# Optimization experiments

Hardware: AMD Instinct MI355X
Metric: run time of the kernel (lower is better)

## Reference

```python
import jax, jax.numpy as jnp
import numpy as np

HID = 32      # STGAT hidden_dim
HEADS = 8
NHID = HID // HEADS  # per-head hidden = 4
NEG_SLOPE = 0.2


def lstm_layer(x, Wih, Whh, bih, bhh):
    # x: (BN, T, H_in); torch gate order i, f, g, o
    BN = x.shape[0]
    H = Whh.shape[1]
    b = bih + bhh

    def step(carry, xt):
        h, c = carry
        z = xt @ Wih.T + h @ Whh.T + b
        i, f, g, o = jnp.split(z, 4, axis=-1)
        c = jax.nn.sigmoid(f) * c + jax.nn.sigmoid(i) * jnp.tanh(g)
        h = jax.nn.sigmoid(o) * jnp.tanh(c)
        return (h, c), h

    h0 = jnp.zeros((BN, H), x.dtype)
    _, ys = jax.lax.scan(step, (h0, h0), jnp.swapaxes(x, 0, 1))
    return jnp.swapaxes(ys, 0, 1)  # (BN, T, H)


def setup_inputs():
    key = jax.random.key(0)
    ks = jax.random.split(key, 16)
    B, N, T_in, F_in = 8, 300, 12, 3
    T_out, F_out = 12, 3
    X = jax.random.normal(ks[0], (B, N, T_in, F_in), jnp.float32)
    adj = (jax.random.uniform(ks[1], (N, N)) < 0.05).astype(jnp.float32)
    A_hat = jnp.maximum(adj, jnp.eye(N, dtype=jnp.float32))  # self-loops

    def init(k, shape, fan):
        return jax.random.normal(k, shape, jnp.float32) / np.float32(np.sqrt(fan))

    W_gat = init(ks[2], (HID, F_in), F_in)          # linear (no bias)
    a_attn = init(ks[3], (2 * NHID,), 2 * NHID)     # attn (no bias), flattened (1, 2*nhid)
    W_ih0 = init(ks[4], (4 * HID, HID), HID)
    W_hh0 = init(ks[5], (4 * HID, HID), HID)
    b_ih0 = init(ks[6], (4 * HID,), HID)
    b_hh0 = init(ks[7], (4 * HID,), HID)
    W_ih1 = init(ks[8], (4 * HID, HID), HID)
    W_hh1 = init(ks[9], (4 * HID, HID), HID)
    b_ih1 = init(ks[10], (4 * HID,), HID)
    b_hh1 = init(ks[11], (4 * HID,), HID)
    fc_W = init(ks[12], (F_out * T_out, HID), HID)
    fc_b = init(ks[13], (F_out * T_out,), HID)
    return {"A_hat": A_hat, "X": X, "W_gat": W_gat, "a_attn": a_attn,
            "W_ih0": W_ih0, "W_hh0": W_hh0, "b_ih0": b_ih0, "b_hh0": b_hh0,
            "W_ih1": W_ih1, "W_hh1": W_hh1, "b_ih1": b_ih1, "b_hh1": b_hh1,
            "fc_W": fc_W, "fc_b": fc_b}


def reference(A_hat, X, W_gat, a_attn, W_ih0, W_hh0, b_ih0, b_hh0,
              W_ih1, W_hh1, b_ih1, b_hh1, fc_W, fc_b):
    B, N, T, F = X.shape
    T_out = fc_W.shape[0] // F  # nums_feature_output == F here

    # --- GAT, vectorized over (batch, timestep) ---
    # g: (B, N, T, HEADS, NHID)
    g = (X @ W_gat.T).reshape(B, N, T, HEADS, NHID)
    a_l, a_r = a_attn[:NHID], a_attn[NHID:]
    # attn(g_concat) = a_l . g_i + a_r . g_j  (exact split of the concat+linear)
    gl = jnp.einsum('bithd,d->bith', g, a_l)
    gr = jnp.einsum('bjthd,d->bjth', g, a_r)
    e = jax.nn.leaky_relu(gl[:, :, None] + gr[:, None, :], NEG_SLOPE)  # (B,i,j,T,H)
    mask = (A_hat == 0)[None, :, :, None, None]
    e = jnp.where(mask, -jnp.inf, e)
    a = jax.nn.softmax(e, axis=2)  # softmax over j (dim=1 of the (i,j,h) tensor)
    h_gat = jnp.einsum('bijth,bjthd->bithd', a, g).reshape(B, N, T, HID)

    # --- 2-layer LSTM over time, per (b, n) sequence ---
    lstm_in = h_gat.reshape(B * N, T, HID)
    h1 = lstm_layer(lstm_in, W_ih0, W_hh0, b_ih0, b_hh0)
    h2 = lstm_layer(h1, W_ih1, W_hh1, b_ih1, b_hh1)
    h_last = h2[:, -1, :]  # (B*N, HID)

    out = h_last @ fc_W.T + fc_b
    return out.reshape(B, N, T_out, F)
```

## Files before the change

### kernel.cpp

```cpp
#include <hip/hip_runtime.h>

typedef __attribute__((ext_vector_type(8))) short s8v;
typedef __attribute__((ext_vector_type(4))) float f4v;

__device__ __forceinline__ float sgm(float x) { return 1.f / (1.f + __expf(-x)); }
__device__ __forceinline__ float tanh_fast(float x) {
    float e = __expf(-2.f * fabsf(x));
    float t = (1.f - e) / (1.f + e);
    return copysignf(t, x);
}
__device__ __forceinline__ void bsplit(float x, short& hi, short& lo) {
    unsigned u = __float_as_uint(x);
    unsigned hb = u & 0xffff0000u;
    hi = (short)(hb >> 16);
    float r = x - __uint_as_float(hb);
    lo = (short)(__float_as_uint(r) >> 16);
}

#define SQ 5

__device__ __forceinline__ f4v zA(const short* vh, const short* vl,
    const s8v (&ah)[2], const s8v (&al)[2], f4v bias, int boff, int g)
{
    s8v bh0 = *(const s8v*)((const char*)vh + boff +      g*16);
    s8v bh1 = *(const s8v*)((const char*)vh + boff + 64 + g*16);
    s8v bl0 = *(const s8v*)((const char*)vl + boff +      g*16);
    s8v bl1 = *(const s8v*)((const char*)vl + boff + 64 + g*16);
    f4v acc = bias;
    acc = __builtin_amdgcn_mfma_f32_16x16x32_bf16(ah[0], bh0, acc, 0, 0, 0);
    acc = __builtin_amdgcn_mfma_f32_16x16x32_bf16(ah[1], bh1, acc, 0, 0, 0);
    acc = __builtin_amdgcn_mfma_f32_16x16x32_bf16(al[0], bh0, acc, 0, 0, 0);
    acc = __builtin_amdgcn_mfma_f32_16x16x32_bf16(al[1], bh1, acc, 0, 0, 0);
    acc = __builtin_amdgcn_mfma_f32_16x16x32_bf16(ah[0], bl0, acc, 0, 0, 0);
    acc = __builtin_amdgcn_mfma_f32_16x16x32_bf16(ah[1], bl1, acc, 0, 0, 0);
    return acc;
}

__global__ __launch_bounds__(512, 4) void k_stgat(
    const float* __restrict__ A,    const float* __restrict__ X,
    const float* __restrict__ Wg,   const float* __restrict__ aat,
    const float* __restrict__ Wih0, const float* __restrict__ Whh0,
    const float* __restrict__ bih0, const float* __restrict__ bhh0,
    const float* __restrict__ Wih1, const float* __restrict__ Whh1,
    const float* __restrict__ bih1, const float* __restrict__ bhh1,
    const float* __restrict__ fcW,  const float* __restrict__ fcb,
    float* __restrict__ out)
{
    __shared__ int   snbr[SQ][64];
    __shared__ int   scnt[SQ];
    __shared__ float shg[SQ*384];
    __shared__ __align__(16) char uarea[43200];
    const int tid  = threadIdx.x;
    const int w    = tid >> 6;
    const int l    = tid & 63;
    const int seq0 = blockIdx.x * SQ;
    const int b    = seq0 / 300, i0 = seq0 - b*300;

    float* Xs = (float*)uarea;

    {
        const float* Xg = X + (size_t)b * 10800;
        for (int x = tid; x < 10800; x += 512) Xs[x] = Xg[x];
    }
    if (w < SQ) {
        int i = i0 + w;
        int c = 0;
        for (int j0 = 0; j0 < 300; j0 += 64) {
            int j = j0 + l;
            bool p = (j < 300) && (A[i*300 + j] != 0.f);
            unsigned long long m = __ballot(p);
            if (p) {
                int pos = __popcll(m & ((1ull << l) - 1ull));
                if (c + pos < 64) snbr[w][c + pos] = j;
            }
            c += __popcll(m);
        }
        if (c > 64) c = 64;
        if (l == 0) scnt[w] = c;
    }

    const int n16 = l & 15;
    const int g   = l >> 4;
    const int cc  = w*4 + g;
    const int arow = (n16 & 3)*32 + w*4 + (n16 >> 2);
    s8v a0h[2], a0l[2], a1h[2], a1l[2];
    {
        const float* s00 = Wih0 + arow*32 + g*8;
        const float* s01 = Whh0 + arow*32 + g*8;
        const float* s10 = Wih1 + arow*32 + g*8;
        const float* s11 = Whh1 + arow*32 + g*8;
        #pragma unroll
        for (int j = 0; j < 8; j++) {
            short hh, ll;
            bsplit(s00[j], hh, ll); a0h[0][j]=hh; a0l[0][j]=ll;
            bsplit(s01[j], hh, ll); a0h[1][j]=hh; a0l[1][j]=ll;
            bsplit(s10[j], hh, ll); a1h[0][j]=hh; a1l[0][j]=ll;
            bsplit(s11[j], hh, ll); a1h[1][j]=hh; a1l[1][j]=ll;
        }
    }
    f4v bias0, bias1;
    #pragma unroll
    for (int r = 0; r < 4; r++) {
        int br = r*32 + cc;
        bias0[r] = bih0[br] + bhh0[br];
        bias1[r] = bih1[br] + bhh1[br];
    }

    __syncthreads();

    {
        const int h = l >> 3, j8 = l & 7, d = j8 & 3;
        float wal0=0.f, wal1=0.f, wal2=0.f, war0=0.f, war1=0.f, war2=0.f;
        #pragma unroll
        for (int dd = 0; dd < 4; dd++) {
            float av = aat[dd], bv = aat[4+dd];
            const float* wr = Wg + (h*4+dd)*3;
            wal0 += wr[0]*av; wal1 += wr[1]*av; wal2 += wr[2]*av;
            war0 += wr[0]*bv; war1 += wr[1]*bv; war2 += wr[2]*bv;
        }
        const float* wp = Wg + (h*4+d)*3;
        float wp0 = wp[0], wp1 = wp[1], wp2 = wp[2];

        for (int u = w; u < SQ*12; u += 8) {
            int us = u / 12, t = u - us*12;
            int i = i0 + us;
            int c = scnt[us];

            const float* Xi = Xs + i*36 + t*3;
            float gl = Xi[0]*wal0 + Xi[1]*wal1 + Xi[2]*wal2;

            float m = -1e30f, s = 0.f, a0 = 0.f, a1 = 0.f, a2 = 0.f;
            for (int kk = j8; kk < c; kk += 8) {
                int j = snbr[us][kk];
                const float* Xj = Xs + j*36 + t*3;
                float y0 = Xj[0], y1 = Xj[1], y2 = Xj[2];
                float e = gl + y0*war0 + y1*war1 + y2*war2;
                e = e > 0.f ? e : 0.2f*e;
                if (e > m) {
                    float sc = __expf(m - e);
                    s = s*sc + 1.f;
                    a0 = a0*sc + y0; a1 = a1*sc + y1; a2 = a2*sc + y2;
                    m = e;
                } else {
                    float wt = __expf(e - m);
                    s += wt;
                    a0 += wt*y0; a1 += wt*y1; a2 += wt*y2;
                }
            }
            #pragma unroll
            for (int off = 1; off <= 4; off <<= 1) {
                float m2 = __shfl_xor(m, off, 64);
                float s2 = __shfl_xor(s, off, 64);
                float b0 = __shfl_xor(a0, off, 64);
                float b1 = __shfl_xor(a1, off, 64);
                float b2 = __shfl_xor(a2, off, 64);
                float mo = fmaxf(m, m2);
                float w1 = __expf(m - mo), w2 = __expf(m2 - mo);
                s = s*w1 + s2*w2;
                a0 = a0*w1 + b0*w2; a1 = a1*w1 + b1*w2; a2 = a2*w1 + b2*w2;
                m = mo;
            }
            if (j8 < 4)
                shg[us*384 + t*32 + h*4 + d] = (a0*wp0 + a1*wp1 + a2*wp2) / s;
        }
    }
    __syncthreads();

    short* vh0 = (short*)uarea;
    short* vl0 = vh0 + 16*72;
    short* vh1 = vl0 + 16*72;
    short* vl1 = vh1 + 16*72;
    float* sh1f = (float*)(vl1 + 16*72);

    for (int x = tid; x < 16*72; x += 512) {
        vh0[x] = 0; vl0[x] = 0; vh1[x] = 0; vl1[x] = 0;
    }
    __syncthreads();
    if (tid < SQ*32) {
        int us = tid >> 5, uc = tid & 31;
        short hh, ll; bsplit(shg[us*384 + uc], hh, ll);
        vh0[us*72 + uc] = hh;  vl0[us*72 + uc] = ll;
    }
    __syncthreads();

    const int boff = n16 * 144;
    float c0 = 0.f, c1 = 0.f;

    {
        f4v z = zA(vh0, vl0, a0h, a0l, bias0, boff, g);
        __syncthreads();
        c0 = sgm(z[1])*c0 + sgm(z[0])*tanh_fast(z[2]);
        float h0v = sgm(z[3])*tanh_fast(c0);
        short hh, ll; bsplit(h0v, hh, ll);
        vh0[n16*72 + 32 + cc] = hh;  vl0[n16*72 + 32 + cc] = ll;
        vh1[n16*72 + cc]      = hh;  vl1[n16*72 + cc]      = ll;
        if (tid < SQ*32) {
            int us = tid >> 5, uc = tid & 31;
            bsplit(shg[us*384 + 32 + uc], hh, ll);
            vh0[us*72 + uc] = hh;  vl0[us*72 + uc] = ll;
        }
        __syncthreads();
    }

    for (int t = 0; t < 12; t++) {
        f4v z1 = zA(vh1, vl1, a1h, a1l, bias1, boff, g);
        f4v z0;
        if (t < 11)
            z0 = zA(vh0, vl0, a0h, a0l, bias0, boff, g);
        __syncthreads();
        c1 = sgm(z1[1])*c1 + sgm(z1[0])*tanh_fast(z1[2]);
        float h1v = sgm(z1[3])*tanh_fast(c1);
        short hh, ll; bsplit(h1v, hh, ll);
        vh1[n16*72 + 32 + cc] = hh;  vl1[n16*72 + 32 + cc] = ll;
        if (t == 11) {
            if (n16 < SQ) sh1f[n16*32 + cc] = h1v;
        } else {
            c0 = sgm(z0[1])*c0 + sgm(z0[0])*tanh_fast(z0[2]);
            float h0v = sgm(z0[3])*tanh_fast(c0);
            bsplit(h0v, hh, ll);
            vh0[n16*72 + 32 + cc] = hh;  vl0[n16*72 + 32 + cc] = ll;
            vh1[n16*72 + cc]      = hh;  vl1[n16*72 + cc]      = ll;
            if (tid < SQ*32 && t + 2 < 12) {
                int us = tid >> 5, uc = tid & 31;
                short h2, l2; bsplit(shg[us*384 + (t+2)*32 + uc], h2, l2);
                vh0[us*72 + uc] = h2;  vl0[us*72 + uc] = l2;
            }
        }
        __syncthreads();
    }

    if (tid < SQ*36) {
        int s = tid / 36, r = tid - s*36;
        float acc = fcb[r];
        #pragma unroll
        for (int c4 = 0; c4 < 8; c4++) {
            float4 uv = *(const float4*)&fcW[r*32 + 4*c4];
            acc += uv.x*sh1f[s*32+4*c4+0] + uv.y*sh1f[s*32+4*c4+1]
                 + uv.z*sh1f[s*32+4*c4+2] + uv.w*sh1f[s*32+4*c4+3];
        }
        out[(seq0 + s)*36 + r] = acc;
    }
}

extern "C" void kernel_launch(void* const* d_in, const int* in_sizes, int n_in,
                              void* d_out, int out_size, void* d_ws, size_t ws_size,
                              hipStream_t stream)
{
    const float* A    = (const float*)d_in[0];
    const float* X    = (const float*)d_in[1];
    const float* Wg   = (const float*)d_in[2];
    const float* aat  = (const float*)d_in[3];
    const float* Wih0 = (const float*)d_in[4];
    const float* Whh0 = (const float*)d_in[5];
    const float* bih0 = (const float*)d_in[6];
    const float* bhh0 = (const float*)d_in[7];
    const float* Wih1 = (const float*)d_in[8];
    const float* Whh1 = (const float*)d_in[9];
    const float* bih1 = (const float*)d_in[10];
    const float* bhh1 = (const float*)d_in[11];
    const float* fcW  = (const float*)d_in[12];
    const float* fcb  = (const float*)d_in[13];
    float* out = (float*)d_out;

    k_stgat<<<480, 512, 0, stream>>>(A, X, Wg, aat,
                                     Wih0, Whh0, bih0, bhh0,
                                     Wih1, Whh1, bih1, bhh1,
                                     fcW, fcb, out);
}
```

Measured before the change: 44.10 us.

## Concentrate LSTM MFMA work on four waves and simplify GAT softmax reductions

Moves the LSTM recurrence onto waves 0-3, each handling two 4-cell groups with doubled MFMA chains, while waves 4-7 stage the next GAT input in parallel. The GAT softmax drops the running-max online update in favour of plain exp sums, reduced with DPP lane moves before a final shuffle. The tanh is replaced by a simpler sigmoid-based formula, and the LSTM weight load is moved after the GAT phase with the GAT wave order reversed. The intent is to cut per-step sync overhead, divergent branches and exp count, at the risk of overflow in the max-free softmax and less parallelism per LSTM step.

```diff
diff --git a/kernel.cpp b/kernel.cpp
--- a/kernel.cpp
+++ b/kernel.cpp
@@ -4,11 +4,7 @@
 typedef __attribute__((ext_vector_type(4))) float f4v;
 
 __device__ __forceinline__ float sgm(float x) { return 1.f / (1.f + __expf(-x)); }
-__device__ __forceinline__ float tanh_fast(float x) {
-    float e = __expf(-2.f * fabsf(x));
-    float t = (1.f - e) / (1.f + e);
-    return copysignf(t, x);
-}
+__device__ __forceinline__ float tanhq(float x) { return 2.f / (1.f + __expf(-2.f*x)) - 1.f; }
 __device__ __forceinline__ void bsplit(float x, short& hi, short& lo) {
     unsigned u = __float_as_uint(x);
     unsigned hb = u & 0xffff0000u;
@@ -16,24 +12,37 @@
     float r = x - __uint_as_float(hb);
     lo = (short)(__float_as_uint(r) >> 16);
 }
+__device__ __forceinline__ float dppadd1(float x) {
+    return x + __uint_as_float(__builtin_amdgcn_mov_dpp(__float_as_uint(x), 0xB1, 0xF, 0xF, true));
+}
+__device__ __forceinline__ float dppadd2(float x) {
+    return x + __uint_as_float(__builtin_amdgcn_mov_dpp(__float_as_uint(x), 0x4E, 0xF, 0xF, true));
+}
 
 #define SQ 5
 
-__device__ __forceinline__ f4v zA(const short* vh, const short* vl,
-    const s8v (&ah)[2], const s8v (&al)[2], f4v bias, int boff, int g)
+__device__ __forceinline__ void zA2(const short* vh, const short* vl,
+    const s8v (&ah)[2][2], const s8v (&al)[2][2], const f4v (&bias)[2],
+    int boff, int g, f4v& dA, f4v& dB)
 {
     s8v bh0 = *(const s8v*)((const char*)vh + boff +      g*16);
     s8v bh1 = *(const s8v*)((const char*)vh + boff + 64 + g*16);
     s8v bl0 = *(const s8v*)((const char*)vl + boff +      g*16);
     s8v bl1 = *(const s8v*)((const char*)vl + boff + 64 + g*16);
-    f4v acc = bias;
-    acc = __builtin_amdgcn_mfma_f32_16x16x32_bf16(ah[0], bh0, acc, 0, 0, 0);
-    acc = __builtin_amdgcn_mfma_f32_16x16x32_bf16(ah[1], bh1, acc, 0, 0, 0);
-    acc = __builtin_amdgcn_mfma_f32_16x16x32_bf16(al[0], bh0, acc, 0, 0, 0);
-    acc = __builtin_amdgcn_mfma_f32_16x16x32_bf16(al[1], bh1, acc, 0, 0, 0);
-    acc = __builtin_amdgcn_mfma_f32_16x16x32_bf16(ah[0], bl0, acc, 0, 0, 0);
-    acc = __builtin_amdgcn_mfma_f32_16x16x32_bf16(ah[1], bl1, acc, 0, 0, 0);
-    return acc;
+    dA = bias[0];
+    dA = __builtin_amdgcn_mfma_f32_16x16x32_bf16(ah[0][0], bh0, dA, 0, 0, 0);
+    dA = __builtin_amdgcn_mfma_f32_16x16x32_bf16(ah[0][1], bh1, dA, 0, 0, 0);
+    dA = __builtin_amdgcn_mfma_f32_16x16x32_bf16(al[0][0], bh0, dA, 0, 0, 0);
+    dA = __builtin_amdgcn_mfma_f32_16x16x32_bf16(al[0][1], bh1, dA, 0, 0, 0);
+    dA = __builtin_amdgcn_mfma_f32_16x16x32_bf16(ah[0][0], bl0, dA, 0, 0, 0);
+    dA = __builtin_amdgcn_mfma_f32_16x16x32_bf16(ah[0][1], bl1, dA, 0, 0, 0);
+    dB = bias[1];
+    dB = __builtin_amdgcn_mfma_f32_16x16x32_bf16(ah[1][0], bh0, dB, 0, 0, 0);
+    dB = __builtin_amdgcn_mfma_f32_16x16x32_bf16(ah[1][1], bh1, dB, 0, 0, 0);
+    dB = __builtin_amdgcn_mfma_f32_16x16x32_bf16(al[1][0], bh0, dB, 0, 0, 0);
+    dB = __builtin_amdgcn_mfma_f32_16x16x32_bf16(al[1][1], bh1, dB, 0, 0, 0);
+    dB = __builtin_amdgcn_mfma_f32_16x16x32_bf16(ah[1][0], bl0, dB, 0, 0, 0);
+    dB = __builtin_amdgcn_mfma_f32_16x16x32_bf16(ah[1][1], bl1, dB, 0, 0, 0);
 }
 
 __global__ __launch_bounds__(512, 4) void k_stgat(
@@ -50,6 +59,7 @@
     __shared__ int   scnt[SQ];
     __shared__ float shg[SQ*384];
     __shared__ __align__(16) char uarea[43200];
+
     const int tid  = threadIdx.x;
     const int w    = tid >> 6;
     const int l    = tid & 63;
@@ -78,50 +88,22 @@
         if (c > 64) c = 64;
         if (l == 0) scnt[w] = c;
     }
-
-    const int n16 = l & 15;
-    const int g   = l >> 4;
-    const int cc  = w*4 + g;
-    const int arow = (n16 & 3)*32 + w*4 + (n16 >> 2);
-    s8v a0h[2], a0l[2], a1h[2], a1l[2];
-    {
-        const float* s00 = Wih0 + arow*32 + g*8;
-        const float* s01 = Whh0 + arow*32 + g*8;
-        const float* s10 = Wih1 + arow*32 + g*8;
-        const float* s11 = Whh1 + arow*32 + g*8;
-        #pragma unroll
-        for (int j = 0; j < 8; j++) {
-            short hh, ll;
-            bsplit(s00[j], hh, ll); a0h[0][j]=hh; a0l[0][j]=ll;
-            bsplit(s01[j], hh, ll); a0h[1][j]=hh; a0l[1][j]=ll;
-            bsplit(s10[j], hh, ll); a1h[0][j]=hh; a1l[0][j]=ll;
-            bsplit(s11[j], hh, ll); a1h[1][j]=hh; a1l[1][j]=ll;
-        }
-    }
-    f4v bias0, bias1;
-    #pragma unroll
-    for (int r = 0; r < 4; r++) {
-        int br = r*32 + cc;
-        bias0[r] = bih0[br] + bhh0[br];
-        bias1[r] = bih1[br] + bhh1[br];
-    }
-
-    __syncthreads();
-
-    {
-        const int h = l >> 3, j8 = l & 7, d = j8 & 3;
+    __syncthreads();
+
+    {
+        const int hh = l >> 3, j8 = l & 7, dd = j8 & 3;
         float wal0=0.f, wal1=0.f, wal2=0.f, war0=0.f, war1=0.f, war2=0.f;
         #pragma unroll
-        for (int dd = 0; dd < 4; dd++) {
-            float av = aat[dd], bv = aat[4+dd];
-            const float* wr = Wg + (h*4+dd)*3;
+        for (int d4 = 0; d4 < 4; d4++) {
+            float av = aat[d4], bv = aat[4+d4];
+            const float* wr = Wg + (hh*4+d4)*3;
             wal0 += wr[0]*av; wal1 += wr[1]*av; wal2 += wr[2]*av;
             war0 += wr[0]*bv; war1 += wr[1]*bv; war2 += wr[2]*bv;
         }
-        const float* wp = Wg + (h*4+d)*3;
+        const float* wp = Wg + (hh*4+dd)*3;
         float wp0 = wp[0], wp1 = wp[1], wp2 = wp[2];
 
-        for (int u = w; u < SQ*12; u += 8) {
+        for (int u = 7 - w; u < SQ*12; u += 8) {
             int us = u / 12, t = u - us*12;
             int i = i0 + us;
             int c = scnt[us];
@@ -129,39 +111,55 @@
             const float* Xi = Xs + i*36 + t*3;
             float gl = Xi[0]*wal0 + Xi[1]*wal1 + Xi[2]*wal2;
 
-            float m = -1e30f, s = 0.f, a0 = 0.f, a1 = 0.f, a2 = 0.f;
+            float s = 0.f, a0 = 0.f, a1 = 0.f, a2 = 0.f;
             for (int kk = j8; kk < c; kk += 8) {
                 int j = snbr[us][kk];
                 const float* Xj = Xs + j*36 + t*3;
                 float y0 = Xj[0], y1 = Xj[1], y2 = Xj[2];
                 float e = gl + y0*war0 + y1*war1 + y2*war2;
                 e = e > 0.f ? e : 0.2f*e;
-                if (e > m) {
-                    float sc = __expf(m - e);
-                    s = s*sc + 1.f;
-                    a0 = a0*sc + y0; a1 = a1*sc + y1; a2 = a2*sc + y2;
-                    m = e;
-                } else {
-                    float wt = __expf(e - m);
-                    s += wt;
-                    a0 += wt*y0; a1 += wt*y1; a2 += wt*y2;
-                }
-            }
+                float wt = __expf(e);
+                s += wt; a0 += wt*y0; a1 += wt*y1; a2 += wt*y2;
+            }
+            s  = dppadd1(s);  a0 = dppadd1(a0); a1 = dppadd1(a1); a2 = dppadd1(a2);
+            s  = dppadd2(s);  a0 = dppadd2(a0); a1 = dppadd2(a1); a2 = dppadd2(a2);
+            s  += __shfl_xor(s, 4, 64);
+            a0 += __shfl_xor(a0, 4, 64);
+            a1 += __shfl_xor(a1, 4, 64);
+            a2 += __shfl_xor(a2, 4, 64);
+            if (j8 < 4)
+                shg[us*384 + t*32 + hh*4 + dd] = (a0*wp0 + a1*wp1 + a2*wp2) / s;
+        }
+    }
+
+    const int n16 = l & 15;
+    const int g   = l >> 4;
+    const int cA  = w*8 + g;
+    const int cB  = w*8 + 4 + g;
+    s8v a0h[2][2], a0l[2][2], a1h[2][2], a1l[2][2];
+    f4v bias0[2], bias1[2];
+    if (w < 4) {
+        #pragma unroll
+        for (int tau = 0; tau < 2; tau++) {
+            const int arow = (n16 & 3)*32 + w*8 + tau*4 + (n16 >> 2);
+            const float* s00 = Wih0 + arow*32 + g*8;
+            const float* s01 = Whh0 + arow*32 + g*8;
+            const float* s10 = Wih1 + arow*32 + g*8;
+            const float* s11 = Whh1 + arow*32 + g*8;
             #pragma unroll
-            for (int off = 1; off <= 4; off <<= 1) {
-                float m2 = __shfl_xor(m, off, 64);
-                float s2 = __shfl_xor(s, off, 64);
-                float b0 = __shfl_xor(a0, off, 64);
-                float b1 = __shfl_xor(a1, off, 64);
-                float b2 = __shfl_xor(a2, off, 64);
-                float mo = fmaxf(m, m2);
-                float w1 = __expf(m - mo), w2 = __expf(m2 - mo);
-                s = s*w1 + s2*w2;
-                a0 = a0*w1 + b0*w2; a1 = a1*w1 + b1*w2; a2 = a2*w1 + b2*w2;
-                m = mo;
-            }
-            if (j8 < 4)
-                shg[us*384 + t*32 + h*4 + d] = (a0*wp0 + a1*wp1 + a2*wp2) / s;
+            for (int j = 0; j < 8; j++) {
+                short hh2, ll2;
+                bsplit(s00[j], hh2, ll2); a0h[tau][0][j]=hh2; a0l[tau][0][j]=ll2;
+                bsplit(s01[j], hh2, ll2); a0h[tau][1][j]=hh2; a0l[tau][1][j]=ll2;
+                bsplit(s10[j], hh2, ll2); a1h[tau][0][j]=hh2; a1l[tau][0][j]=ll2;
+                bsplit(s11[j], hh2, ll2); a1h[tau][1][j]=hh2; a1l[tau][1][j]=ll2;
+            }
+            const int cell = w*8 + tau*4 + g;
+            #pragma unroll
+            for (int r = 0; r < 4; r++) {
+                bias0[tau][r] = bih0[r*32+cell] + bhh0[r*32+cell];
+                bias1[tau][r] = bih1[r*32+cell] + bhh1[r*32+cell];
+            }
         }
     }
     __syncthreads();
@@ -172,59 +170,74 @@
     short* vl1 = vh1 + 16*72;
     float* sh1f = (float*)(vl1 + 16*72);
 
-    for (int x = tid; x < 16*72; x += 512) {
-        vh0[x] = 0; vl0[x] = 0; vh1[x] = 0; vl1[x] = 0;
-    }
-    __syncthreads();
-    if (tid < SQ*32) {
-        int us = tid >> 5, uc = tid & 31;
-        short hh, ll; bsplit(shg[us*384 + uc], hh, ll);
-        vh0[us*72 + uc] = hh;  vl0[us*72 + uc] = ll;
+    {
+        unsigned* vz = (unsigned*)uarea;
+        for (int x = tid; x < 2304; x += 512) vz[x] = 0;
+    }
+    __syncthreads();
+    if (tid >= 256 && tid < 416) {
+        int us = (tid - 256) >> 5, uc = tid & 31;
+        short hh2, ll2; bsplit(shg[us*384 + uc], hh2, ll2);
+        vh0[us*72 + uc] = hh2;  vl0[us*72 + uc] = ll2;
     }
     __syncthreads();
 
     const int boff = n16 * 144;
-    float c0 = 0.f, c1 = 0.f;
-
-    {
-        f4v z = zA(vh0, vl0, a0h, a0l, bias0, boff, g);
-        __syncthreads();
-        c0 = sgm(z[1])*c0 + sgm(z[0])*tanh_fast(z[2]);
-        float h0v = sgm(z[3])*tanh_fast(c0);
-        short hh, ll; bsplit(h0v, hh, ll);
-        vh0[n16*72 + 32 + cc] = hh;  vl0[n16*72 + 32 + cc] = ll;
-        vh1[n16*72 + cc]      = hh;  vl1[n16*72 + cc]      = ll;
-        if (tid < SQ*32) {
-            int us = tid >> 5, uc = tid & 31;
-            bsplit(shg[us*384 + 32 + uc], hh, ll);
-            vh0[us*72 + uc] = hh;  vl0[us*72 + uc] = ll;
+    float c0A = 0.f, c0B = 0.f, c1A = 0.f, c1B = 0.f;
+
+    auto cellup = [&](f4v z, float& cs) -> float {
+        cs = sgm(z[1])*cs + sgm(z[0])*tanhq(z[2]);
+        return sgm(z[3])*tanhq(cs);
+    };
+    auto wr_h0 = [&](float hv, int c) {
+        short hh2, ll2; bsplit(hv, hh2, ll2);
+        vh0[n16*72 + 32 + c] = hh2;  vl0[n16*72 + 32 + c] = ll2;
+        vh1[n16*72 + c]      = hh2;  vl1[n16*72 + c]      = ll2;
+    };
+    auto wr_h1 = [&](float hv, int c) {
+        short hh2, ll2; bsplit(hv, hh2, ll2);
+        vh1[n16*72 + 32 + c] = hh2;  vl1[n16*72 + 32 + c] = ll2;
+    };
+
+    {
+        f4v zpA, zpB;
+        if (w < 4) zA2(vh0, vl0, a0h, a0l, bias0, boff, g, zpA, zpB);
+        __syncthreads();
+        if (w < 4) {
+            wr_h0(cellup(zpA, c0A), cA);
+            wr_h0(cellup(zpB, c0B), cB);
+        }
+        if (tid >= 256 && tid < 416) {
+            int us = (tid - 256) >> 5, uc = tid & 31;
+            short hh2, ll2; bsplit(shg[us*384 + 32 + uc], hh2, ll2);
+            vh0[us*72 + uc] = hh2;  vl0[us*72 + uc] = ll2;
         }
         __syncthreads();
     }
 
     for (int t = 0; t < 12; t++) {
-        f4v z1 = zA(vh1, vl1, a1h, a1l, bias1, boff, g);
-        f4v z0;
-        if (t < 11)
-            z0 = zA(vh0, vl0, a0h, a0l, bias0, boff, g);
-        __syncthreads();
-        c1 = sgm(z1[1])*c1 + sgm(z1[0])*tanh_fast(z1[2]);
-        float h1v = sgm(z1[3])*tanh_fast(c1);
-        short hh, ll; bsplit(h1v, hh, ll);
-        vh1[n16*72 + 32 + cc] = hh;  vl1[n16*72 + 32 + cc] = ll;
-        if (t == 11) {
-            if (n16 < SQ) sh1f[n16*32 + cc] = h1v;
-        } else {
-            c0 = sgm(z0[1])*c0 + sgm(z0[0])*tanh_fast(z0[2]);
-            float h0v = sgm(z0[3])*tanh_fast(c0);
-            bsplit(h0v, hh, ll);
-            vh0[n16*72 + 32 + cc] = hh;  vl0[n16*72 + 32 + cc] = ll;
-            vh1[n16*72 + cc]      = hh;  vl1[n16*72 + cc]      = ll;
-            if (tid < SQ*32 && t + 2 < 12) {
-                int us = tid >> 5, uc = tid & 31;
-                short h2, l2; bsplit(shg[us*384 + (t+2)*32 + uc], h2, l2);
-                vh0[us*72 + uc] = h2;  vl0[us*72 + uc] = l2;
-            }
+        f4v z1A, z1B, z0A, z0B;
+        if (w < 4) {
+            zA2(vh1, vl1, a1h, a1l, bias1, boff, g, z1A, z1B);
+            if (t < 11)
+                zA2(vh0, vl0, a0h, a0l, bias0, boff, g, z0A, z0B);
+        }
+        __syncthreads();
+        if (w < 4) {
+            float h1a = cellup(z1A, c1A);
+            float h1b = cellup(z1B, c1B);
+            wr_h1(h1a, cA);  wr_h1(h1b, cB);
+            if (t == 11) {
+                if (n16 < SQ) { sh1f[n16*32 + cA] = h1a; sh1f[n16*32 + cB] = h1b; }
+            } else {
+                wr_h0(cellup(z0A, c0A), cA);
+                wr_h0(cellup(z0B, c0B), cB);
+            }
+        }
+        if (tid >= 256 && tid < 416 && t < 10) {
+            int us = (tid - 256) >> 5, uc = tid & 31;
+            short hh2, ll2; bsplit(shg[us*384 + (t+2)*32 + uc], hh2, ll2);
+            vh0[us*72 + uc] = hh2;  vl0[us*72 + uc] = ll2;
         }
         __syncthreads();
     }
```

After: 36.82 us. 1.2x faster.
